# Performance work log

Hardware: AMD Instinct MI355X
Metric: run time of the kernel (lower is better)

The kernel has to match this reference:

```python
import jax, jax.numpy as jnp
import numpy as np

# Static module config (must match init_kwargs / input_specs)
C, HEADS, POINTS, LEVELS = 256, 8, 8, 2
H, W = 128, 128           # BEV grid per agent/level
NQ = H * W                # num_query = H*W
DH = C // HEADS           # per-head dim


def setup_inputs() -> dict:
    key = jax.random.key(0)
    ks = jax.random.split(key, 12)
    s = 0.02
    return {
        "query": jax.random.normal(ks[0], (1, NQ, C), jnp.float32),
        "query_pos": jax.random.normal(ks[1], (1, NQ, C), jnp.float32),
        "value": jax.random.normal(ks[2], (LEVELS, NQ, C), jnp.float32),
        "reference_points": jax.random.uniform(ks[3], (1, NQ, LEVELS, 2), jnp.float32),
        "spatial_shapes": jnp.full((LEVELS, 2), H, dtype=jnp.int32),
        "W_off": jax.random.normal(ks[4], (C, LEVELS * HEADS * POINTS * 2), jnp.float32) * s,
        "b_off": jax.random.normal(ks[5], (LEVELS * HEADS * POINTS * 2,), jnp.float32) * s,
        "W_attn": jax.random.normal(ks[6], (C, LEVELS * HEADS * POINTS), jnp.float32) * s,
        "b_attn": jax.random.normal(ks[7], (LEVELS * HEADS * POINTS,), jnp.float32) * s,
        "W_val": jax.random.normal(ks[8], (C, C), jnp.float32) * s,
        "b_val": jax.random.normal(ks[9], (C,), jnp.float32) * s,
        "W_out": jax.random.normal(ks[10], (C, C), jnp.float32) * s,
        "b_out": jax.random.normal(ks[11], (C,), jnp.float32) * s,
    }


def _bilinear(img, x, y):
    """grid_sample-style bilinear, align_corners=False, zero padding.
    img: (H, W, D); x, y: (...) pixel-space coords. Returns (..., D)."""
    Hh, Ww = img.shape[0], img.shape[1]
    x0f, y0f = jnp.floor(x), jnp.floor(y)
    x0, y0 = x0f.astype(jnp.int32), y0f.astype(jnp.int32)
    x1, y1 = x0 + 1, y0 + 1
    wx1, wy1 = x - x0f, y - y0f
    wx0, wy0 = 1.0 - wx1, 1.0 - wy1

    def gather(yy, xx):
        valid = (yy >= 0) & (yy < Hh) & (xx >= 0) & (xx < Ww)
        g = img[jnp.clip(yy, 0, Hh - 1), jnp.clip(xx, 0, Ww - 1)]
        return jnp.where(valid[..., None], g, 0.0)

    return (gather(y0, x0) * (wy0 * wx0)[..., None]
            + gather(y0, x1) * (wy0 * wx1)[..., None]
            + gather(y1, x0) * (wy1 * wx0)[..., None]
            + gather(y1, x1) * (wy1 * wx1)[..., None])


_sample_heads = jax.vmap(_bilinear, in_axes=(0, 0, 0))  # over heads


def reference(query, query_pos, value, reference_points, spatial_shapes,
              W_off, b_off, W_attn, b_attn, W_val, b_val, W_out, b_out):
    identity = query                                        # (1, NQ, C)
    q = (query + query_pos)[0]                              # (NQ, C), bs=1

    v = value @ W_val + b_val                               # (L, NQ, C)
    v = v.reshape(LEVELS, H, W, HEADS, DH)                  # per-level feature maps

    off = (q @ W_off + b_off).reshape(NQ, HEADS, LEVELS, POINTS, 2)
    attn = (q @ W_attn + b_attn).reshape(NQ, HEADS, LEVELS * POINTS)
    attn = jax.nn.softmax(attn, axis=-1).reshape(NQ, HEADS, LEVELS, POINTS)

    # offset_normalizer = (W, H) per level
    norm = jnp.stack([spatial_shapes[:, 1], spatial_shapes[:, 0]], -1).astype(q.dtype)  # (L, 2)
    # sampling_locations in normalized [0,1] coords: (NQ, HEADS, LEVELS, POINTS, 2)
    loc = reference_points[0][:, None, :, None, :] + off / norm[None, None, :, None, :]

    out = jnp.zeros((NQ, HEADS, DH), dtype=q.dtype)
    for l in range(LEVELS):
        img_l = jnp.transpose(v[l], (2, 0, 1, 3))           # (HEADS, H, W, DH)
        # align_corners=False: px = x_norm * W - 0.5
        xl = jnp.transpose(loc[:, :, l, :, 0], (1, 0, 2)) * W - 0.5  # (HEADS, NQ, POINTS)
        yl = jnp.transpose(loc[:, :, l, :, 1], (1, 0, 2)) * H - 0.5
        sampled = _sample_heads(img_l, xl, yl)              # (HEADS, NQ, POINTS, DH)
        out = out + jnp.einsum('hqpd,qhp->qhd', sampled, attn[:, :, l, :])

    out = out.reshape(NQ, C) @ W_out + b_out                # (NQ, C)
    return out[None] + identity                             # dropout is identity (eval / p=0)
```

## Files before the change

### kernel.cpp

```cpp
#include <hip/hip_runtime.h>
#include <hip/hip_bf16.h>
#include <math.h>

#define NQ     16384
#define CDIM   256
#define NHEADS 8
#define NPTS   8
#define NLVL   2
#define HH     128
#define WWID   128
#define DHEAD  32
#define NCAT   384

#define PW        130
#define CELLB     32
#define ROWB      (PW * CELLB)
#define MAPB      (PW * PW * CELLB)
#define V2BYTES   (NLVL * NHEADS * MAPB)
#define MEMSET_BLKS 2113

typedef __bf16 bf16_t;
typedef __bf16 bf16x8 __attribute__((ext_vector_type(8)));
typedef float  f32x4  __attribute__((ext_vector_type(4)));
typedef float  f32x2  __attribute__((ext_vector_type(2)));

typedef __attribute__((address_space(1))) const uint32_t gau32;
typedef __attribute__((address_space(3))) uint32_t lau32;

__device__ __forceinline__ bf16_t f2b(float f) { return (bf16_t)f; }

__global__ __launch_bounds__(256) void prep_k(const float* __restrict__ W_val,
                                              const float* __restrict__ W_off,
                                              const float* __restrict__ W_attn,
                                              const float* __restrict__ W_out,
                                              unsigned char* __restrict__ v2,
                                              bf16_t* __restrict__ Wt_val,
                                              bf16_t* __restrict__ Wt_qa,
                                              bf16_t* __restrict__ Wt_out) {
    const int b = blockIdx.x;
    if (b < MEMSET_BLKS) {
        size_t off = ((size_t)b * 256 + threadIdx.x) * 16;
        if (off < V2BYTES)
            *reinterpret_cast<uint4*>(v2 + off) = make_uint4(0, 0, 0, 0);
        return;
    }
    const int tb = b - MEMSET_BLKS;
    const float* W; bf16_t* Wt; int N, t;
    if (tb < 64)       { W = W_val;  Wt = Wt_val;            N = 256; t = tb;       }
    else if (tb < 128) { W = W_off;  Wt = Wt_qa;             N = 256; t = tb - 64;  }
    else if (tb < 160) { W = W_attn; Wt = Wt_qa + 256 * 256; N = 128; t = tb - 128; }
    else               { W = W_out;  Wt = Wt_out;            N = 256; t = tb - 160; }
    const int ntn = N >> 5;
    const int k0 = (t / ntn) * 32, n0 = (t % ntn) * 32;
    const int tx = threadIdx.x & 31, ty = threadIdx.x >> 5;
    __shared__ float s[32][33];
#pragma unroll
    for (int i = 0; i < 4; ++i)
        s[ty + 8 * i][tx] = W[(size_t)(k0 + ty + 8 * i) * N + n0 + tx];
    __syncthreads();
#pragma unroll
    for (int i = 0; i < 4; ++i)
        Wt[(size_t)(n0 + ty + 8 * i) * 256 + k0 + tx] = f2b(s[tx][ty + 8 * i]);
}

template <int A_MODE, bool OUT_BF16, bool ADD_SRC, bool PERM_V>
__device__ __forceinline__ void gemm_body(bf16_t (&As)[128][64], bf16_t (&Bs)[128][64],
                                          int bidx, int bidy,
                                          const void* __restrict__ Aptr,
                                          const void* __restrict__ Aptr2,
                                          const bf16_t* __restrict__ Bt,
                                          const float* __restrict__ bias,
                                          const float* __restrict__ bias2,
                                          int Nsplit,
                                          const float* __restrict__ addsrc,
                                          void* __restrict__ Cout,
                                          int N, int K) {
    const int tid  = threadIdx.x;
    const int wave = tid >> 6;
    const int lane = tid & 63;
    const int rowBase = bidy * 128;
    const int colBase = bidx * 128;
    const int wm = (wave & 1) * 64;
    const int wn = (wave >> 1) * 64;
    const int fr = lane & 15;
    const int fq = lane >> 4;

    f32x4 acc[4][4] = {};

    const int lrow = lane >> 3;
    const int scol = ((lane & 7) ^ lrow) * 8;

    for (int k0 = 0; k0 < K; k0 += 64) {
        __syncthreads();
        if (A_MODE != 0) {
            const int r = tid >> 1, c = tid & 1;
            const float* ap = (const float*)Aptr + (size_t)(rowBase + r) * K + k0 + c * 32;
            const float* ap2 = (A_MODE == 2)
                ? (const float*)Aptr2 + (size_t)(rowBase + r) * K + k0 + c * 32 : nullptr;
#pragma unroll
            for (int u = 0; u < 4; ++u) {
                float4 f0 = *reinterpret_cast<const float4*>(ap + u * 8);
                float4 f1 = *reinterpret_cast<const float4*>(ap + u * 8 + 4);
                if (A_MODE == 2) {
                    float4 g0 = *reinterpret_cast<const float4*>(ap2 + u * 8);
                    float4 g1 = *reinterpret_cast<const float4*>(ap2 + u * 8 + 4);
                    f0.x += g0.x; f0.y += g0.y; f0.z += g0.z; f0.w += g0.w;
                    f1.x += g1.x; f1.y += g1.y; f1.z += g1.z; f1.w += g1.w;
                }
                bf16x8 bv;
                bv[0] = f2b(f0.x); bv[1] = f2b(f0.y); bv[2] = f2b(f0.z); bv[3] = f2b(f0.w);
                bv[4] = f2b(f1.x); bv[5] = f2b(f1.y); bv[6] = f2b(f1.z); bv[7] = f2b(f1.w);
                const int gp = ((c * 4 + u) ^ (r & 7)) * 8;
                *reinterpret_cast<bf16x8*>(&As[r][gp]) = bv;
            }
        } else {
            const bf16_t* Abf = (const bf16_t*)Aptr;
#pragma unroll
            for (int t = 0; t < 4; ++t) {
                const bf16_t* src =
                    Abf + (size_t)(rowBase + wave * 32 + t * 8 + lrow) * K + k0 + scol;
                __builtin_amdgcn_global_load_lds((gau32*)src,
                                                 (lau32*)&As[wave * 32 + t * 8][0],
                                                 16, 0, 0);
            }
        }
#pragma unroll
        for (int t = 0; t < 4; ++t) {
            const bf16_t* src =
                Bt + (size_t)(colBase + wave * 32 + t * 8 + lrow) * K + k0 + scol;
            __builtin_amdgcn_global_load_lds((gau32*)src,
                                             (lau32*)&Bs[wave * 32 + t * 8][0],
                                             16, 0, 0);
        }
        __syncthreads();
#pragma unroll
        for (int ks = 0; ks < 2; ++ks) {
            const int gk = ((ks * 4 + fq) ^ (fr & 7)) * 8;
            bf16x8 af[4], bfr[4];
#pragma unroll
            for (int i = 0; i < 4; ++i)
                af[i] = *reinterpret_cast<const bf16x8*>(&As[wm + i * 16 + fr][gk]);
#pragma unroll
            for (int j = 0; j < 4; ++j)
                bfr[j] = *reinterpret_cast<const bf16x8*>(&Bs[wn + j * 16 + fr][gk]);
#pragma unroll
            for (int i = 0; i < 4; ++i)
#pragma unroll
                for (int j = 0; j < 4; ++j)
                    acc[i][j] = __builtin_amdgcn_mfma_f32_16x16x32_bf16(af[i], bfr[j],
                                                                        acc[i][j], 0, 0, 0);
        }
    }

#pragma unroll
    for (int j = 0; j < 4; ++j) {
        const int col = colBase + wn + j * 16 + fr;
        const float bv = (col < Nsplit) ? bias[col] : bias2[col - Nsplit];
#pragma unroll
        for (int i = 0; i < 4; ++i) {
#pragma unroll
            for (int r = 0; r < 4; ++r) {
                const int row = rowBase + wm + i * 16 + fq * 4 + r;
                float vv = acc[i][j][r] + bv;
                if (ADD_SRC) vv += addsrc[(size_t)row * N + col];
                if (PERM_V) {
                    const int l = row >> 14, cell = row & 16383;
                    const int y = cell >> 7, x = cell & 127;
                    const size_t dst = (size_t)(l * NHEADS + (col >> 5)) * MAPB
                                     + (size_t)(y + 1) * ROWB + (x + 1) * CELLB
                                     + (col & 31);
                    const uint32_t pk = __builtin_amdgcn_cvt_pk_fp8_f32(vv, vv, 0, false);
                    ((unsigned char*)Cout)[dst] = (unsigned char)(pk & 0xff);
                } else if (OUT_BF16) {
                    ((bf16_t*)Cout)[(size_t)row * N + col] = f2b(vv);
                } else {
                    ((float*)Cout)[(size_t)row * N + col] = vv;
                }
            }
        }
    }
}

__global__ __launch_bounds__(256, 3) void fused_proj_k(const float* __restrict__ value,
                                                       const float* __restrict__ query,
                                                       const float* __restrict__ query_pos,
                                                       const bf16_t* __restrict__ Wt_val,
                                                       const bf16_t* __restrict__ Wt_qa,
                                                       const float* __restrict__ b_val,
                                                       const float* __restrict__ b_off,
                                                       const float* __restrict__ b_attn,
                                                       unsigned char* __restrict__ v2,
                                                       float* __restrict__ cbuf) {
    __shared__ __align__(16) bf16_t As[128][64];
    __shared__ __align__(16) bf16_t Bs[128][64];
    const int b = blockIdx.x;
    if (b < 512) {
        const int bidy = (b >> 4) * 8 + (b & 7);
        const int bidx = (b >> 3) & 1;
        gemm_body<1, true, false, true>(As, Bs, bidx, bidy, value, nullptr,
                                        Wt_val, b_val, b_val, 256, nullptr, v2,
                                        CDIM, CDIM);
    } else {
        const int b2 = b - 512;
        const int bidy = (b2 / 24) * 8 + (b2 & 7);
        const int bidx = (b2 >> 3) % 3;
        gemm_body<2, false, false, false>(As, Bs, bidx, bidy, query, query_pos,
                                          Wt_qa, b_off, b_attn, 256, nullptr, cbuf,
                                          NCAT, CDIM);
    }
}

__global__ __launch_bounds__(256, 3) void outproj_k(const bf16_t* __restrict__ tmp,
                                                    const bf16_t* __restrict__ Wt_out,
                                                    const float* __restrict__ b_out,
                                                    const float* __restrict__ query,
                                                    float* __restrict__ out) {
    __shared__ __align__(16) bf16_t As[128][64];
    __shared__ __align__(16) bf16_t Bs[128][64];
    const int b = blockIdx.x;
    const int bidy = (b >> 4) * 8 + (b & 7);
    const int bidx = (b >> 3) & 1;
    gemm_body<0, false, true, false>(As, Bs, bidx, bidy, tmp, nullptr,
                                     Wt_out, b_out, b_out, 256, query, out,
                                     CDIM, CDIM);
}

__device__ __forceinline__ void acc_tap(uint2 u, float w, f32x2* acc2) {
    acc2[0] += __builtin_amdgcn_cvt_pk_f32_fp8((int)u.x, false) * w;
    acc2[1] += __builtin_amdgcn_cvt_pk_f32_fp8((int)u.x, true)  * w;
    acc2[2] += __builtin_amdgcn_cvt_pk_f32_fp8((int)u.y, false) * w;
    acc2[3] += __builtin_amdgcn_cvt_pk_f32_fp8((int)u.y, true)  * w;
}

__global__ __launch_bounds__(256) void sample_k(const unsigned char* __restrict__ v2,
                                                const float* __restrict__ cbuf,
                                                const float* __restrict__ refp,
                                                bf16_t* __restrict__ tmp) {
    const int b    = blockIdx.x;
    const int h    = b & 7;
    const int qblk = b >> 3;
    const int tid  = threadIdx.x;
    const int qloc = tid >> 2;
    const int ck   = tid & 3;
    const int q    = qblk * 64 + qloc;

    const float* qrow = cbuf + (size_t)q * NCAT;
    const float4 rp = *reinterpret_cast<const float4*>(refp + (size_t)q * 4);

    const float* attp = qrow + 256 + h * 16;
    float4 A0 = *reinterpret_cast<const float4*>(attp);
    float4 A1 = *reinterpret_cast<const float4*>(attp + 4);
    float4 A2 = *reinterpret_cast<const float4*>(attp + 8);
    float4 A3 = *reinterpret_cast<const float4*>(attp + 12);
    float e[16] = {A0.x, A0.y, A0.z, A0.w, A1.x, A1.y, A1.z, A1.w,
                   A2.x, A2.y, A2.z, A2.w, A3.x, A3.y, A3.z, A3.w};
    float m = e[0];
#pragma unroll
    for (int i = 1; i < 16; ++i) m = fmaxf(m, e[i]);
    float s = 0.f;
#pragma unroll
    for (int i = 0; i < 16; ++i) { e[i] = __expf(e[i] - m); s += e[i]; }
    const float inv = 1.f / s;
#pragma unroll
    for (int i = 0; i < 16; ++i) e[i] *= inv;

    f32x2 acc2[4] = {{0.f, 0.f}, {0.f, 0.f}, {0.f, 0.f}, {0.f, 0.f}};

#pragma unroll
    for (int l = 0; l < NLVL; ++l) {
        const float bx = (l == 0 ? rp.x : rp.z) * (float)WWID - 0.5f;
        const float by = (l == 0 ? rp.y : rp.w) * (float)HH - 0.5f;
        const unsigned char* base = v2 + (size_t)(l * NHEADS + h) * MAPB
                                       + 131 * CELLB + ck * 8;
        const float* offp = qrow + h * 32 + l * 16;

        float4 o0 = *reinterpret_cast<const float4*>(offp);
        float4 o1 = *reinterpret_cast<const float4*>(offp + 4);
        float4 o2 = *reinterpret_cast<const float4*>(offp + 8);
        float4 o3 = *reinterpret_cast<const float4*>(offp + 12);
        const float ox[8] = {o0.x, o0.z, o1.x, o1.z, o2.x, o2.z, o3.x, o3.z};
        const float oy[8] = {o0.y, o0.w, o1.y, o1.w, o2.y, o2.w, o3.y, o3.w};

#pragma unroll
        for (int p = 0; p < NPTS; ++p) {
            const float px = bx + ox[p];
            const float py = by + oy[p];
            const float w  = e[l * 8 + p];
            const float x0f = floorf(px), y0f = floorf(py);
            const int x0 = (int)x0f, y0 = (int)y0f;
            const float wx1 = px - x0f, wy1 = py - y0f;
            const float wx0 = 1.f - wx1, wy0 = 1.f - wy1;
            const int x0c = min(max(x0, -1), 128);
            const int x1c = min(max(x0 + 1, -1), 128);
            const int y0c = min(max(y0, -1), 128);
            const int y1c = min(max(y0 + 1, -1), 128);
            const unsigned char* r0 = base + y0c * ROWB;
            const unsigned char* r1 = base + y1c * ROWB;
            uint2 u00 = *reinterpret_cast<const uint2*>(r0 + x0c * CELLB);
            uint2 u10 = *reinterpret_cast<const uint2*>(r0 + x1c * CELLB);
            uint2 u01 = *reinterpret_cast<const uint2*>(r1 + x0c * CELLB);
            uint2 u11 = *reinterpret_cast<const uint2*>(r1 + x1c * CELLB);
            const float wy0w = w * wy0, wy1w = w * wy1;
            acc_tap(u00, wy0w * wx0, acc2);
            acc_tap(u10, wy0w * wx1, acc2);
            acc_tap(u01, wy1w * wx0, acc2);
            acc_tap(u11, wy1w * wx1, acc2);
        }
    }

    bf16x8 ov;
#pragma unroll
    for (int i = 0; i < 4; ++i) {
        ov[2 * i]     = f2b(acc2[i].x);
        ov[2 * i + 1] = f2b(acc2[i].y);
    }
    *reinterpret_cast<bf16x8*>(tmp + (size_t)q * CDIM + h * DHEAD + ck * 8) = ov;
}

extern "C" void kernel_launch(void* const* d_in, const int* in_sizes, int n_in,
                              void* d_out, int out_size, void* d_ws, size_t ws_size,
                              hipStream_t stream) {
    const float* query     = (const float*)d_in[0];
    const float* query_pos = (const float*)d_in[1];
    const float* value     = (const float*)d_in[2];
    const float* refp      = (const float*)d_in[3];
    const float* W_off  = (const float*)d_in[5];
    const float* b_off  = (const float*)d_in[6];
    const float* W_attn = (const float*)d_in[7];
    const float* b_attn = (const float*)d_in[8];
    const float* W_val  = (const float*)d_in[9];
    const float* b_val  = (const float*)d_in[10];
    const float* W_out  = (const float*)d_in[11];
    const float* b_out  = (const float*)d_in[12];
    float* out = (float*)d_out;

    char* ws = (char*)d_ws;
    unsigned char* v2 = (unsigned char*)(ws);
    float*  cbuf    = (float*)(ws + 8654848);
    bf16_t* tmp     = (bf16_t*)(ws + 33820672);
    bf16_t* Wt_val  = (bf16_t*)(ws + 42209280);
    bf16_t* Wt_qa   = (bf16_t*)(ws + 42340352);
    bf16_t* Wt_out  = (bf16_t*)(ws + 42536960);

    prep_k<<<MEMSET_BLKS + 224, 256, 0, stream>>>(W_val, W_off, W_attn, W_out,
                                                  v2, Wt_val, Wt_qa, Wt_out);
    fused_proj_k<<<896, 256, 0, stream>>>(value, query, query_pos,
                                          Wt_val, Wt_qa, b_val, b_off, b_attn,
                                          v2, cbuf);
    sample_k<<<2048, 256, 0, stream>>>(v2, cbuf, refp, tmp);
    outproj_k<<<256, 256, 0, stream>>>(tmp, Wt_out, b_out, query, out);
}
```

Before: 197.4 us.

## Permute value-projection weight columns to store packed 4-byte fp8 outputs

Reorders the W_val transpose so each lane's four MFMA output columns map to four consecutive head-dim channels. The value GEMM epilogue can then pack four fp8 values into one 32-bit store instead of issuing single-byte scattered stores. The byte-write traffic into the padded value map is meant to shrink. Launch bounds for the fused projection kernel also rise to 4 blocks per SM, which may squeeze registers and cause spills.

```diff
diff --git a/kernel.cpp b/kernel.cpp
--- a/kernel.cpp
+++ b/kernel.cpp
@@ -45,8 +45,8 @@
         return;
     }
     const int tb = b - MEMSET_BLKS;
-    const float* W; bf16_t* Wt; int N, t;
-    if (tb < 64)       { W = W_val;  Wt = Wt_val;            N = 256; t = tb;       }
+    const float* W; bf16_t* Wt; int N, t; bool permute = false;
+    if (tb < 64)       { W = W_val;  Wt = Wt_val;            N = 256; t = tb;       permute = true; }
     else if (tb < 128) { W = W_off;  Wt = Wt_qa;             N = 256; t = tb - 64;  }
     else if (tb < 160) { W = W_attn; Wt = Wt_qa + 256 * 256; N = 128; t = tb - 128; }
     else               { W = W_out;  Wt = Wt_out;            N = 256; t = tb - 160; }
@@ -59,8 +59,11 @@
         s[ty + 8 * i][tx] = W[(size_t)(k0 + ty + 8 * i) * N + n0 + tx];
     __syncthreads();
 #pragma unroll
-    for (int i = 0; i < 4; ++i)
-        Wt[(size_t)(n0 + ty + 8 * i) * 256 + k0 + tx] = f2b(s[tx][ty + 8 * i]);
+    for (int i = 0; i < 4; ++i) {
+        const int n = n0 + ty + 8 * i;
+        const int p = permute ? ((n & ~63) | ((n & 3) << 4) | ((n & 63) >> 2)) : n;
+        Wt[(size_t)p * 256 + k0 + tx] = f2b(s[tx][ty + 8 * i]);
+    }
 }
 
 template <int A_MODE, bool OUT_BF16, bool ADD_SRC, bool PERM_V>
@@ -152,6 +155,32 @@
         }
     }
 
+    if (PERM_V) {
+        const int lbase = colBase + wn + fr * 4;
+        const float bv0 = bias[lbase], bv1 = bias[lbase + 1];
+        const float bv2 = bias[lbase + 2], bv3 = bias[lbase + 3];
+        const int hh = (lbase >> 5) & 7;
+        const int dbase = lbase & 31;
+        unsigned char* outp = (unsigned char*)Cout;
+#pragma unroll
+        for (int i = 0; i < 4; ++i) {
+#pragma unroll
+            for (int r = 0; r < 4; ++r) {
+                const int row = rowBase + wm + i * 16 + fq * 4 + r;
+                const int lv = row >> 14, cell = row & 16383;
+                const int y = cell >> 7, x = cell & 127;
+                uint32_t pk = __builtin_amdgcn_cvt_pk_fp8_f32(
+                    acc[i][0][r] + bv0, acc[i][1][r] + bv1, 0, false);
+                pk = (uint32_t)__builtin_amdgcn_cvt_pk_fp8_f32(
+                    acc[i][2][r] + bv2, acc[i][3][r] + bv3, pk, true);
+                *reinterpret_cast<uint32_t*>(
+                    outp + (size_t)(lv * NHEADS + hh) * MAPB
+                         + (size_t)(y + 1) * ROWB + (x + 1) * CELLB + dbase) = pk;
+            }
+        }
+        return;
+    }
+
 #pragma unroll
     for (int j = 0; j < 4; ++j) {
         const int col = colBase + wn + j * 16 + fr;
@@ -163,25 +192,16 @@
                 const int row = rowBase + wm + i * 16 + fq * 4 + r;
                 float vv = acc[i][j][r] + bv;
                 if (ADD_SRC) vv += addsrc[(size_t)row * N + col];
-                if (PERM_V) {
-                    const int l = row >> 14, cell = row & 16383;
-                    const int y = cell >> 7, x = cell & 127;
-                    const size_t dst = (size_t)(l * NHEADS + (col >> 5)) * MAPB
-                                     + (size_t)(y + 1) * ROWB + (x + 1) * CELLB
-                                     + (col & 31);
-                    const uint32_t pk = __builtin_amdgcn_cvt_pk_fp8_f32(vv, vv, 0, false);
-                    ((unsigned char*)Cout)[dst] = (unsigned char)(pk & 0xff);
-                } else if (OUT_BF16) {
+                if (OUT_BF16)
                     ((bf16_t*)Cout)[(size_t)row * N + col] = f2b(vv);
-                } else {
+                else
                     ((float*)Cout)[(size_t)row * N + col] = vv;
-                }
             }
         }
     }
 }
 
-__global__ __launch_bounds__(256, 3) void fused_proj_k(const float* __restrict__ value,
+__global__ __launch_bounds__(256, 4) void fused_proj_k(const float* __restrict__ value,
                                                        const float* __restrict__ query,
                                                        const float* __restrict__ query_pos,
                                                        const bf16_t* __restrict__ Wt_val,
```

After: 198.5 us. Within noise of the previous version (+0.6%).
